# Optimization experiments

Hardware: AMD Instinct MI355X
Metric: run time of the kernel (lower is better)

The kernel has to match this reference:

```python
import jax, jax.numpy as jnp
import numpy as np

N = 100000      # nodes
E = 3200000     # edges (before self-loops)
IN = 1          # input feature dim
H1, C = 4, 8    # layer1: 4 heads x 8 channels; layer2: 1 head x 8 channels
NEG_SLOPE = 0.2


def setup_inputs() -> dict:
    key = jax.random.key(0)
    ks = jax.random.split(key, 10)
    x = jax.random.normal(ks[0], (N, IN), jnp.float32)
    edge_index = jax.random.randint(ks[1], (2, E), 0, N, dtype=jnp.int32)
    # layer 1 params (GATConv(1, 8, heads=4))
    W1 = jax.random.normal(ks[2], (IN, H1 * C), jnp.float32) * 0.5
    a_src1 = jax.random.normal(ks[3], (H1, C), jnp.float32) * 0.5
    a_dst1 = jax.random.normal(ks[4], (H1, C), jnp.float32) * 0.5
    b1 = jnp.zeros((H1 * C,), jnp.float32)
    # layer 2 params (GATConv(32, 8, heads=1))
    W2 = jax.random.normal(ks[5], (H1 * C, C), jnp.float32) * 0.2
    a_src2 = jax.random.normal(ks[6], (1, C), jnp.float32) * 0.5
    a_dst2 = jax.random.normal(ks[7], (1, C), jnp.float32) * 0.5
    b2 = jnp.zeros((C,), jnp.float32)
    return {"x": x, "edge_index": edge_index, "W1": W1, "a_src1": a_src1,
            "a_dst1": a_dst1, "b1": b1, "W2": W2, "a_src2": a_src2,
            "a_dst2": a_dst2, "b2": b2}


def _gat_layer(x, src, dst, W, a_s, a_d, b, heads, ch):
    # Linear transform per head: [N, heads, ch]
    h = (x @ W).reshape(-1, heads, ch)
    # per-node attention logits
    al_s = jnp.einsum('nhc,hc->nh', h, a_s)  # [N, H]
    al_d = jnp.einsum('nhc,hc->nh', h, a_d)  # [N, H]
    # per-edge logits (message src -> dst)
    e = jax.nn.leaky_relu(al_s[src] + al_d[dst], NEG_SLOPE)  # [E', H]
    # segment softmax over incoming edges of each dst node
    m = jax.ops.segment_max(e, dst, num_segments=N)          # [N, H]
    e = jnp.exp(e - m[dst])
    s = jax.ops.segment_sum(e, dst, num_segments=N)          # [N, H]
    alpha = e / s[dst]                                       # [E', H]
    # weighted scatter-add aggregation
    out = jax.ops.segment_sum(h[src] * alpha[:, :, None], dst, num_segments=N)
    return out.reshape(N, heads * ch) + b


def reference(x, edge_index, W1, a_src1, a_dst1, b1, W2, a_src2, a_dst2, b2):
    loops = jnp.arange(N, dtype=edge_index.dtype)
    src = jnp.concatenate([edge_index[0], loops])  # add self-loops (PyG default)
    dst = jnp.concatenate([edge_index[1], loops])
    h = _gat_layer(x, src, dst, W1, a_src1, a_dst1, b1, H1, C)
    h = jax.nn.relu(h)
    out = _gat_layer(h, src, dst, W2, a_src2, a_dst2, b2, 1, C)
    return out
```

## Files before the change

### kernel.cpp

```cpp
#include <hip/hip_runtime.h>
#include <hip/hip_bf16.h>

#define NEG_SLOPE 0.2f
#define CAPS 8192
#define CAPG 8192
#define CAPA 81920


__global__ void init_cc(int* __restrict__ curA, int* __restrict__ curB,
                        const float* __restrict__ W1,
                        const float* __restrict__ as1,
                        const float* __restrict__ ad1,
                        float* __restrict__ consts) {
    int t = threadIdx.x;
    if (t < 8) {
        int h = t & 3;
        const float* a = (t < 4) ? as1 : ad1;
        float s = 0.f;
        #pragma unroll
        for (int c = 0; c < 8; ++c)
            s += W1[h * 8 + c] * a[h * 8 + c];
        consts[t] = s;
    }
    if (t < 64) curA[t] = t * CAPA;
    curB[t] = t << 13;
}

__global__ void scatterA(const int* __restrict__ ei, int* __restrict__ curA,
                         unsigned int* __restrict__ bufA, int E) {
    __shared__ int cnt[64];
    __shared__ int basel[64];
    int t = threadIdx.x;
    int chunk = (E + gridDim.x - 1) / gridDim.x;
    int lo = blockIdx.x * chunk;
    int hi = min(E, lo + chunk);
    const int* dei = ei + E;
    if (t < 64) cnt[t] = 0;
    __syncthreads();
    bool vec = ((E & 3) == 0);
    int lo4 = (lo + 3) & ~3;
    int end4 = hi & ~3;
    if (vec && end4 > lo4) {
        for (int e = lo + t; e < lo4; e += 1024) atomicAdd(&cnt[dei[e] >> 11], 1);
        const int4* dei4 = (const int4*)dei;
        for (int v = (lo4 >> 2) + t; v < (end4 >> 2); v += 1024) {
            int4 d = dei4[v];
            atomicAdd(&cnt[d.x >> 11], 1); atomicAdd(&cnt[d.y >> 11], 1);
            atomicAdd(&cnt[d.z >> 11], 1); atomicAdd(&cnt[d.w >> 11], 1);
        }
        for (int e = end4 + t; e < hi; e += 1024) atomicAdd(&cnt[dei[e] >> 11], 1);
    } else {
        for (int e = lo + t; e < hi; e += 1024) atomicAdd(&cnt[dei[e] >> 11], 1);
    }
    __syncthreads();
    if (t < 64) {
        int c = cnt[t];
        basel[t] = c ? (atomicAdd(&curA[t], c) - t * CAPA) : 0;
        cnt[t] = 0;
    }
    __syncthreads();
    if (vec && end4 > lo4) {
        for (int e = lo + t; e < lo4; e += 1024) {
            int s = ei[e], d = dei[e]; int sp = d >> 11;
            int off = basel[sp] + atomicAdd(&cnt[sp], 1);
            if (off < CAPA) bufA[sp * CAPA + off] = (unsigned)s | ((unsigned)(d & 2047) << 17);
        }
        const int4* sei4 = (const int4*)ei;
        const int4* dei4 = (const int4*)dei;
        for (int v = (lo4 >> 2) + t; v < (end4 >> 2); v += 1024) {
            int4 sv = sei4[v]; int4 dv = dei4[v];
            int s0 = dv.x >> 11, s1 = dv.y >> 11, s2 = dv.z >> 11, s3 = dv.w >> 11;
            int o0 = basel[s0] + atomicAdd(&cnt[s0], 1);
            if (o0 < CAPA) bufA[s0 * CAPA + o0] = (unsigned)sv.x | ((unsigned)(dv.x & 2047) << 17);
            int o1 = basel[s1] + atomicAdd(&cnt[s1], 1);
            if (o1 < CAPA) bufA[s1 * CAPA + o1] = (unsigned)sv.y | ((unsigned)(dv.y & 2047) << 17);
            int o2 = basel[s2] + atomicAdd(&cnt[s2], 1);
            if (o2 < CAPA) bufA[s2 * CAPA + o2] = (unsigned)sv.z | ((unsigned)(dv.z & 2047) << 17);
            int o3 = basel[s3] + atomicAdd(&cnt[s3], 1);
            if (o3 < CAPA) bufA[s3 * CAPA + o3] = (unsigned)sv.w | ((unsigned)(dv.w & 2047) << 17);
        }
        for (int e = end4 + t; e < hi; e += 1024) {
            int s = ei[e], d = dei[e]; int sp = d >> 11;
            int off = basel[sp] + atomicAdd(&cnt[sp], 1);
            if (off < CAPA) bufA[sp * CAPA + off] = (unsigned)s | ((unsigned)(d & 2047) << 17);
        }
    } else {
        for (int e = lo + t; e < hi; e += 1024) {
            int s = ei[e], d = dei[e]; int sp = d >> 11;
            int off = basel[sp] + atomicAdd(&cnt[sp], 1);
            if (off < CAPA) bufA[sp * CAPA + off] = (unsigned)s | ((unsigned)(d & 2047) << 17);
        }
    }
}

__global__ void scatterB(const int* __restrict__ curA, int* __restrict__ curB,
                         const unsigned int* __restrict__ bufA,
                         unsigned int* __restrict__ pairs) {
    __shared__ int cnt[16];
    __shared__ int basel[16];
    int t = threadIdx.x;
    int sp = blockIdx.x >> 3;
    int part = blockIdx.x & 7;
    int base = sp * CAPA;
    int fill = min(curA[sp] - base, CAPA);
    if (fill <= 0) return;
    int lo = (fill * part) >> 3;
    int hi = (fill * (part + 1)) >> 3;
    for (int c0 = lo; c0 < hi; c0 += 8192) {
        int cend = min(hi, c0 + 8192);
        if (t < 16) cnt[t] = 0;
        __syncthreads();
        for (int i = c0 + t; i < cend; i += 1024)
            atomicAdd(&cnt[(bufA[base + i] >> 24) & 15], 1);
        __syncthreads();
        if (t < 16) {
            int c = cnt[t];
            int bkg = (sp << 4) + t;
            basel[t] = c ? (atomicAdd(&curB[bkg], c) - (bkg << 13)) : 0;
            cnt[t] = 0;
        }
        __syncthreads();
        for (int i = c0 + t; i < cend; i += 1024) {
            unsigned p = bufA[base + i];
            int b16 = (p >> 24) & 15;
            int off = basel[b16] + atomicAdd(&cnt[b16], 1);
            if (off < CAPG) pairs[(((sp << 4) + b16) << 13) + off] = p & 0x00FFFFFFu;
        }
        __syncthreads();
    }
}

__global__ __launch_bounds__(512, 8)
void l1_comb(const float* __restrict__ x,
             const int* __restrict__ curB,
             const unsigned int* __restrict__ pairs,
             unsigned int* __restrict__ gsorted, int* __restrict__ bmeta,
             const float* __restrict__ consts,
             const float* __restrict__ W1, const float* __restrict__ b1,
             const float* __restrict__ W2,
             const float* __restrict__ as2, const float* __restrict__ ad2,
             float* __restrict__ h2, float* __restrict__ als2,
             float* __restrict__ ald2, int N) {
    __shared__ unsigned sbuf[CAPS];
    __shared__ int hcnt[128], offs[128], hcur[128];
    __shared__ float xl[128];
    int t = threadIdx.x;
    int bk = blockIdx.x;
    int node0 = bk << 7;
    int nw = min(128, N - node0);
    if (t < 128) xl[t] = (t < nw) ? x[node0 + t] : 0.f;
    float S[4], D[4];
    #pragma unroll
    for (int h = 0; h < 4; ++h) { S[h] = consts[h]; D[h] = consts[4 + h]; }
    int base = bk << 13;
    int clen = min(curB[bk] - base, CAPG);
    int clen6 = min(clen, 6144);
    int g = t >> 2, jj = t & 3;
    unsigned pr[12];
    #pragma unroll
    for (int k = 0; k < 12; ++k) {
        int idx = t + (k << 9);
        pr[k] = (idx < clen6) ? pairs[base + idx] : 0xFFFFFFFFu;
    }
    if (t < 128) hcnt[t] = 0;
    __syncthreads();
    #pragma unroll
    for (int k = 0; k < 12; ++k)
        if (pr[k] != 0xFFFFFFFFu) atomicAdd(&hcnt[pr[k] >> 17], 1);
    for (int idx = 6144 + t; idx < clen; idx += 512)
        atomicAdd(&hcnt[pairs[base + idx] >> 17], 1);
    __syncthreads();
    if (t < 64) {
        int h0 = hcnt[2 * t], h1 = hcnt[2 * t + 1];
        int s = h0 + h1, sc_ = s;
        #pragma unroll
        for (int o = 1; o < 64; o <<= 1) {
            int u = __shfl_up(sc_, o);
            if (t >= o) sc_ += u;
        }
        int excl = sc_ - s;
        offs[2 * t] = excl;          hcur[2 * t] = excl;
        offs[2 * t + 1] = excl + h0; hcur[2 * t + 1] = excl + h0;
    }
    __syncthreads();
    #pragma unroll
    for (int k = 0; k < 12; ++k)
        if (pr[k] != 0xFFFFFFFFu) {
            int loc = atomicAdd(&hcur[pr[k] >> 17], 1);
            sbuf[loc] = pr[k];
        }
    for (int idx = 6144 + t; idx < clen; idx += 512) {
        unsigned p = pairs[base + idx];
        int loc = atomicAdd(&hcur[p >> 17], 1);
        sbuf[loc] = p;
    }
    __syncthreads();
    for (int i = t; i < clen; i += 512) gsorted[base + i] = sbuf[i];
    if (t < 128) bmeta[(bk << 7) + t] = offs[t] | (hcnt[t] << 14);
    float xd = xl[g];
    float sacc[4] = {0.f, 0.f, 0.f, 0.f};
    float tacc[4] = {0.f, 0.f, 0.f, 0.f};
    int st = offs[g], en = st + hcnt[g];
    int i = st + jj;
    while (i + 28 < en) {
        unsigned p0 = sbuf[i],      p1 = sbuf[i + 4],  p2 = sbuf[i + 8],
                 p3 = sbuf[i + 12], p4 = sbuf[i + 16], p5 = sbuf[i + 20],
                 p6 = sbuf[i + 24], p7 = sbuf[i + 28];
        float x0 = x[p0 & 131071u], x1 = x[p1 & 131071u];
        float x2 = x[p2 & 131071u], x3 = x[p3 & 131071u];
        float x4 = x[p4 & 131071u], x5 = x[p5 & 131071u];
        float x6 = x[p6 & 131071u], x7 = x[p7 & 131071u];
        float xs_[8] = {x0, x1, x2, x3, x4, x5, x6, x7};
        #pragma unroll
        for (int q = 0; q < 8; ++q) {
            float xs = xs_[q];
            #pragma unroll
            for (int h = 0; h < 4; ++h) {
                float v = xs * S[h] + xd * D[h];
                v = (v > 0.f) ? v : NEG_SLOPE * v;
                float w = __expf(v);
                sacc[h] += w;
                tacc[h] = fmaf(w, xs, tacc[h]);
            }
        }
        i += 32;
    }
    for (; i < en; i += 4) {
        float xs = x[sbuf[i] & 131071u];
        #pragma unroll
        for (int h = 0; h < 4; ++h) {
            float v = xs * S[h] + xd * D[h];
            v = (v > 0.f) ? v : NEG_SLOPE * v;
            float w = __expf(v);
            sacc[h] += w;
            tacc[h] = fmaf(w, xs, tacc[h]);
        }
    }
    #pragma unroll
    for (int h = 0; h < 4; ++h) {
        sacc[h] += __shfl_xor(sacc[h], 1); sacc[h] += __shfl_xor(sacc[h], 2);
        tacc[h] += __shfl_xor(tacc[h], 1); tacc[h] += __shfl_xor(tacc[h], 2);
    }
    if (jj == 0 && g < nw) {
        int n = node0 + g;
        float xn = xd;
        float o[8];
        #pragma unroll
        for (int c = 0; c < 8; ++c) o[c] = 0.f;
        #pragma unroll
        for (int h = 0; h < 4; ++h) {
            float v = xn * (S[h] + D[h]);
            v = (v > 0.f) ? v : NEG_SLOPE * v;
            float ww = __expf(v);
            float s1 = ww + sacc[h];
            float t1 = ww * xn + tacc[h];
            float tt = t1 / s1;
            #pragma unroll
            for (int c = 0; c < 8; ++c) {
                float rr = fmaxf(tt * W1[h * 8 + c] + b1[h * 8 + c], 0.f);
                #pragma unroll
                for (int c2 = 0; c2 < 8; ++c2) o[c2] += rr * W2[(h * 8 + c) * 8 + c2];
            }
        }
        float as = 0.f, ad = 0.f;
        #pragma unroll
        for (int c = 0; c < 8; ++c) { as += o[c] * as2[c]; ad += o[c] * ad2[c]; }
        float4* hv = (float4*)&h2[(size_t)n * 8];
        hv[0] = make_float4(o[0], o[1], o[2], o[3]);
        hv[1] = make_float4(o[4], o[5], o[6], o[7]);
        als2[n] = as;
        ald2[n] = ad;
    }
}

__global__ __launch_bounds__(512, 8)
void l2_comb(const unsigned int* __restrict__ gsorted,
             const int* __restrict__ bmeta,
             const float* __restrict__ als2, const float* __restrict__ ald2,
             const float* __restrict__ h2, const float* __restrict__ b2,
             float* __restrict__ out, int N) {
    __shared__ float adl[128];
    int t = threadIdx.x;
    int bk = blockIdx.x;
    int node0 = bk << 7;
    int nw = min(128, N - node0);
    if (t < 128) adl[t] = (t < nw) ? ald2[node0 + t] : 0.f;
    __syncthreads();
    int g = t >> 2, j2 = t & 3;
    if (g >= nw) return;
    int base = bk << 13;
    int pk = bmeta[(bk << 7) + g];
    int st = pk & 16383, cgn = pk >> 14;
    const unsigned* run = gsorted + base + st;
    const float2* h2f2 = (const float2*)h2;
    float adv = adl[g];
    float sw = 0.f, acc0 = 0.f, acc1 = 0.f;
    int i = 0;
    while (i + 8 <= cgn) {
        unsigned p0 = run[i],     p1 = run[i + 1], p2 = run[i + 2], p3 = run[i + 3],
                 p4 = run[i + 4], p5 = run[i + 5], p6 = run[i + 6], p7 = run[i + 7];
        int s0 = (int)(p0 & 131071u), s1 = (int)(p1 & 131071u);
        int s2 = (int)(p2 & 131071u), s3 = (int)(p3 & 131071u);
        int s4 = (int)(p4 & 131071u), s5 = (int)(p5 & 131071u);
        int s6 = (int)(p6 & 131071u), s7 = (int)(p7 & 131071u);
        float a0 = als2[s0], a1 = als2[s1], a2 = als2[s2], a3 = als2[s3];
        float a4 = als2[s4], a5 = als2[s5], a6 = als2[s6], a7 = als2[s7];
        float2 h0 = h2f2[s0 * 4 + j2], h1 = h2f2[s1 * 4 + j2];
        float2 h2v = h2f2[s2 * 4 + j2], h3 = h2f2[s3 * 4 + j2];
        float2 h4 = h2f2[s4 * 4 + j2], h5 = h2f2[s5 * 4 + j2];
        float2 h6 = h2f2[s6 * 4 + j2], h7 = h2f2[s7 * 4 + j2];
        float aa[8] = {a0, a1, a2, a3, a4, a5, a6, a7};
        float2 hh[8] = {h0, h1, h2v, h3, h4, h5, h6, h7};
        #pragma unroll
        for (int q = 0; q < 8; ++q) {
            float v = aa[q] + adv;
            v = (v > 0.f) ? v : NEG_SLOPE * v;
            float w = __expf(v);
            sw += w;
            acc0 = fmaf(w, hh[q].x, acc0);
            acc1 = fmaf(w, hh[q].y, acc1);
        }
        i += 8;
    }
    for (; i < cgn; ++i) {
        unsigned p = run[i];
        int s = (int)(p & 131071u);
        float a = als2[s];
        float2 hv = h2f2[s * 4 + j2];
        float v = a + adv;
        v = (v > 0.f) ? v : NEG_SLOPE * v;
        float w = __expf(v);
        sw += w;
        acc0 = fmaf(w, hv.x, acc0);
        acc1 = fmaf(w, hv.y, acc1);
    }
    int n = node0 + g;
    float v = als2[n] + adv;
    v = (v > 0.f) ? v : NEG_SLOPE * v;
    float ww = __expf(v);
    float2 hs = h2f2[n * 4 + j2];
    float inv = 1.f / (sw + ww);
    float2* ov = (float2*)&out[(size_t)n * 8];
    ov[j2] = make_float2((acc0 + ww * hs.x) * inv + b2[2 * j2],
                         (acc1 + ww * hs.y) * inv + b2[2 * j2 + 1]);
}


__global__ void prep_consts(const float* __restrict__ W1,
                            const float* __restrict__ as1,
                            const float* __restrict__ ad1,
                            float* __restrict__ consts) {
    int t = threadIdx.x;
    if (t >= 8) return;
    int h = t & 3;
    const float* a = (t < 4) ? as1 : ad1;
    float s = 0.f;
    #pragma unroll
    for (int c = 0; c < 8; ++c)
        s += W1[h * 8 + c] * a[h * 8 + c];
    consts[t] = s;
}

__global__ void edge_pass1(const int* __restrict__ ei, const float* __restrict__ x,
                           const float* __restrict__ consts,
                           float* __restrict__ s1, float* __restrict__ t1, int E, int N) {
    int e = blockIdx.x * blockDim.x + threadIdx.x;
    if (e >= E + N) return;
    int src, dst;
    if (e < E) { src = ei[e]; dst = ei[E + e]; }
    else       { src = dst = e - E; }
    float xs = x[src], xd = x[dst];
    #pragma unroll
    for (int h = 0; h < 4; ++h) {
        float v = xs * consts[h] + xd * consts[4 + h];
        v = (v > 0.f) ? v : NEG_SLOPE * v;
        float w = __expf(v);
        atomicAdd(&s1[dst * 4 + h], w);
        atomicAdd(&t1[dst * 4 + h], w * xs);
    }
}

__global__ void node_mid(const float* __restrict__ s1, const float* __restrict__ t1,
                         const float* __restrict__ W1, const float* __restrict__ b1,
                         const float* __restrict__ W2,
                         const float* __restrict__ as2, const float* __restrict__ ad2,
                         float* __restrict__ h2, float* __restrict__ als2,
                         float* __restrict__ ald2, int N) {
    int n = blockIdx.x * blockDim.x + threadIdx.x;
    if (n >= N) return;
    float o[8];
    #pragma unroll
    for (int c = 0; c < 8; ++c) o[c] = 0.f;
    #pragma unroll
    for (int h = 0; h < 4; ++h) {
        float t = t1[n * 4 + h] / s1[n * 4 + h];
        #pragma unroll
        for (int c = 0; c < 8; ++c) {
            float r = fmaxf(t * W1[h * 8 + c] + b1[h * 8 + c], 0.f);
            #pragma unroll
            for (int c2 = 0; c2 < 8; ++c2) o[c2] += r * W2[(h * 8 + c) * 8 + c2];
        }
    }
    float as = 0.f, ad = 0.f;
    #pragma unroll
    for (int c = 0; c < 8; ++c) { h2[n * 8 + c] = o[c]; as += o[c] * as2[c]; ad += o[c] * ad2[c]; }
    als2[n] = as; ald2[n] = ad;
}

__global__ void edge_pass2(const int* __restrict__ ei, const float* __restrict__ als2,
                           const float* __restrict__ ald2, const float* __restrict__ h2,
                           float* __restrict__ s2, float* __restrict__ acc2, int E, int N) {
    int e = blockIdx.x * blockDim.x + threadIdx.x;
    if (e >= E + N) return;
    int src, dst;
    if (e < E) { src = ei[e]; dst = ei[E + e]; }
    else       { src = dst = e - E; }
    float v = als2[src] + ald2[dst];
    v = (v > 0.f) ? v : NEG_SLOPE * v;
    float w = __expf(v);
    atomicAdd(&s2[dst], w);
    const float4* hs = (const float4*)&h2[src * 8];
    float4 a = hs[0], bq = hs[1];
    float* acc = &acc2[dst * 8];
    atomicAdd(&acc[0], w * a.x);  atomicAdd(&acc[1], w * a.y);
    atomicAdd(&acc[2], w * a.z);  atomicAdd(&acc[3], w * a.w);
    atomicAdd(&acc[4], w * bq.x); atomicAdd(&acc[5], w * bq.y);
    atomicAdd(&acc[6], w * bq.z); atomicAdd(&acc[7], w * bq.w);
}

__global__ void node_out(const float* __restrict__ s2, const float* __restrict__ acc2,
                         const float* __restrict__ b2, float* __restrict__ out, int N) {
    int i = blockIdx.x * blockDim.x + threadIdx.x;
    if (i >= N * 8) return;
    out[i] = acc2[i] / s2[i >> 3] + b2[i & 7];
}


extern "C" void kernel_launch(void* const* d_in, const int* in_sizes, int n_in,
                              void* d_out, int out_size, void* d_ws, size_t ws_size,
                              hipStream_t stream) {
    const float* x   = (const float*)d_in[0];
    const int*   ei  = (const int*)d_in[1];
    const float* W1  = (const float*)d_in[2];
    const float* as1 = (const float*)d_in[3];
    const float* ad1 = (const float*)d_in[4];
    const float* b1  = (const float*)d_in[5];
    const float* W2  = (const float*)d_in[6];
    const float* as2 = (const float*)d_in[7];
    const float* ad2 = (const float*)d_in[8];
    const float* b2  = (const float*)d_in[9];
    float* out = (float*)d_out;

    const int N = in_sizes[0];
    const int E = in_sizes[1] / 2;
    const int NBK = (N + 127) >> 7;

    float* ws = (float*)d_ws;
    size_t need = ((size_t)16 + 64 + 1024 + 131072 + 10 * (size_t)N
                   + 2 * (size_t)1024 * CAPG + (size_t)64 * CAPA) * sizeof(float);

    if (N <= 131072 && ws_size >= need) {
        float*    consts  = ws;
        int*      curA    = (int*)(ws + 16);
        int*      curB    = curA + 64;
        int*      bmeta   = curB + 1024;
        float*    als2    = (float*)(bmeta + 131072);
        float*    ald2    = als2 + N;
        float*    h2      = ald2 + N;
        unsigned* pairs   = (unsigned*)(h2 + 8 * (size_t)N);
        unsigned* gsorted = pairs + (size_t)1024 * CAPG;
        unsigned* bufA    = gsorted + (size_t)1024 * CAPG;

        init_cc<<<1, 1024, 0, stream>>>(curA, curB, W1, as1, ad1, consts);
        scatterA<<<256, 1024, 0, stream>>>(ei, curA, bufA, E);
        scatterB<<<512, 1024, 0, stream>>>(curA, curB, bufA, pairs);
        l1_comb<<<NBK, 512, 0, stream>>>(x, curB, pairs, gsorted, bmeta, consts,
                                         W1, b1, W2, as2, ad2, h2, als2, ald2, N);
        l2_comb<<<NBK, 512, 0, stream>>>(gsorted, bmeta, als2, ald2, h2, b2, out, N);
    } else {
        float* consts = ws;
        float* s1   = ws + 16;
        float* t1   = s1 + 4 * (size_t)N;
        float* h2   = t1 + 4 * (size_t)N;
        float* als2 = h2 + 8 * (size_t)N;
        float* ald2 = als2 + (size_t)N;
        float* s2   = ald2 + (size_t)N;
        float* acc2 = s2 + (size_t)N;

        hipMemsetAsync(ws, 0, (16 + 8 * (size_t)N) * sizeof(float), stream);
        hipMemsetAsync(s2, 0, 9 * (size_t)N * sizeof(float), stream);
        prep_consts<<<1, 64, 0, stream>>>(W1, as1, ad1, consts);
        int total = E + N;
        edge_pass1<<<(total + 255) / 256, 256, 0, stream>>>(ei, x, consts, s1, t1, E, N);
        node_mid<<<(N + 255) / 256, 256, 0, stream>>>(s1, t1, W1, b1, W2, as2, ad2, h2, als2, ald2, N);
        edge_pass2<<<(total + 255) / 256, 256, 0, stream>>>(ei, als2, ald2, h2, s2, acc2, E, N);
        node_out<<<(N * 8 + 255) / 256, 256, 0, stream>>>(s2, acc2, b2, out, N);
    }
}
```

Baseline: 187.0 us.

## Vectorize pair loads/stores and restructure l2_comb with LDS-staged runs and float4 gathers

In l1_comb, the pair loads and the write-back of sorted pairs now use 128-bit uint4 accesses. In l2_comb, the block's sorted edge run is first copied into shared memory with uint4 loads. Each group of four lanes now splits into two edge streams, each lane gathering a float4 half of the source feature row, and the partial sums are combined with a shuffle. This is meant to cut the number of global memory transactions and per-edge index loads. In exchange it uses 32KB of LDS per block, which may lower occupancy, and it assumes 16-byte alignment.

```diff
diff --git a/kernel.cpp b/kernel.cpp
--- a/kernel.cpp
+++ b/kernel.cpp
@@ -157,10 +157,20 @@
     int clen6 = min(clen, 6144);
     int g = t >> 2, jj = t & 3;
     unsigned pr[12];
-    #pragma unroll
-    for (int k = 0; k < 12; ++k) {
-        int idx = t + (k << 9);
-        pr[k] = (idx < clen6) ? pairs[base + idx] : 0xFFFFFFFFu;
+    const uint4* pairs4 = (const uint4*)(pairs + base);
+    #pragma unroll
+    for (int k = 0; k < 3; ++k) {
+        int w4 = t + (k << 9);
+        int wi = w4 << 2;
+        if (wi + 3 < clen6) {
+            uint4 v = pairs4[w4];
+            pr[4 * k]     = v.x; pr[4 * k + 1] = v.y;
+            pr[4 * k + 2] = v.z; pr[4 * k + 3] = v.w;
+        } else {
+            #pragma unroll
+            for (int m = 0; m < 4; ++m)
+                pr[4 * k + m] = (wi + m < clen6) ? pairs[base + wi + m] : 0xFFFFFFFFu;
+        }
     }
     if (t < 128) hcnt[t] = 0;
     __syncthreads();
@@ -195,7 +205,14 @@
         sbuf[loc] = p;
     }
     __syncthreads();
-    for (int i = t; i < clen; i += 512) gsorted[base + i] = sbuf[i];
+    {
+        int clen4 = clen & ~3;
+        for (int i = t << 2; i < clen4; i += 2048) {
+            uint4 v = *(const uint4*)&sbuf[i];
+            *(uint4*)&gsorted[base + i] = v;
+        }
+        for (int i = clen4 + t; i < clen; i += 512) gsorted[base + i] = sbuf[i];
+    }
     if (t < 128) bmeta[(bk << 7) + t] = offs[t] | (hcnt[t] << 14);
     float xd = xl[g];
     float sacc[4] = {0.f, 0.f, 0.f, 0.f};
@@ -274,75 +291,104 @@
 }
 
 __global__ __launch_bounds__(512, 8)
-void l2_comb(const unsigned int* __restrict__ gsorted,
+void l2_comb(const int* __restrict__ curB,
+             const unsigned int* __restrict__ gsorted,
              const int* __restrict__ bmeta,
              const float* __restrict__ als2, const float* __restrict__ ald2,
              const float* __restrict__ h2, const float* __restrict__ b2,
              float* __restrict__ out, int N) {
+    __shared__ unsigned runl[CAPS];
     __shared__ float adl[128];
     int t = threadIdx.x;
     int bk = blockIdx.x;
     int node0 = bk << 7;
     int nw = min(128, N - node0);
     if (t < 128) adl[t] = (t < nw) ? ald2[node0 + t] : 0.f;
-    __syncthreads();
-    int g = t >> 2, j2 = t & 3;
+    int base = bk << 13;
+    int clen = min(curB[bk] - base, CAPG);
+    {
+        int clen4 = clen & ~3;
+        const uint4* g4 = (const uint4*)(gsorted + base);
+        for (int i = t << 2; i < clen4; i += 2048) {
+            uint4 v = g4[i >> 2];
+            *(uint4*)&runl[i] = v;
+        }
+        for (int i = clen4 + t; i < clen; i += 512) runl[i] = gsorted[base + i];
+    }
+    __syncthreads();
+    int g = t >> 2, j = t & 3;
+    int jh = j & 1;
+    int jp = j >> 1;
     if (g >= nw) return;
-    int base = bk << 13;
     int pk = bmeta[(bk << 7) + g];
     int st = pk & 16383, cgn = pk >> 14;
-    const unsigned* run = gsorted + base + st;
-    const float2* h2f2 = (const float2*)h2;
+    const unsigned* run = runl + st;
     float adv = adl[g];
-    float sw = 0.f, acc0 = 0.f, acc1 = 0.f;
-    int i = 0;
-    while (i + 8 <= cgn) {
-        unsigned p0 = run[i],     p1 = run[i + 1], p2 = run[i + 2], p3 = run[i + 3],
-                 p4 = run[i + 4], p5 = run[i + 5], p6 = run[i + 6], p7 = run[i + 7];
-        int s0 = (int)(p0 & 131071u), s1 = (int)(p1 & 131071u);
-        int s2 = (int)(p2 & 131071u), s3 = (int)(p3 & 131071u);
-        int s4 = (int)(p4 & 131071u), s5 = (int)(p5 & 131071u);
-        int s6 = (int)(p6 & 131071u), s7 = (int)(p7 & 131071u);
-        float a0 = als2[s0], a1 = als2[s1], a2 = als2[s2], a3 = als2[s3];
-        float a4 = als2[s4], a5 = als2[s5], a6 = als2[s6], a7 = als2[s7];
-        float2 h0 = h2f2[s0 * 4 + j2], h1 = h2f2[s1 * 4 + j2];
-        float2 h2v = h2f2[s2 * 4 + j2], h3 = h2f2[s3 * 4 + j2];
-        float2 h4 = h2f2[s4 * 4 + j2], h5 = h2f2[s5 * 4 + j2];
-        float2 h6 = h2f2[s6 * 4 + j2], h7 = h2f2[s7 * 4 + j2];
-        float aa[8] = {a0, a1, a2, a3, a4, a5, a6, a7};
-        float2 hh[8] = {h0, h1, h2v, h3, h4, h5, h6, h7};
-        #pragma unroll
-        for (int q = 0; q < 8; ++q) {
+    int co = jh << 2;
+    float4 acc = make_float4(0.f, 0.f, 0.f, 0.f);
+    float sw = 0.f;
+    int k = 0;
+    while (2 * k + 8 <= cgn) {
+        unsigned q0 = run[2 * k + jp];
+        unsigned q1 = run[2 * k + 2 + jp];
+        unsigned q2 = run[2 * k + 4 + jp];
+        unsigned q3 = run[2 * k + 6 + jp];
+        size_t r0 = (size_t)(q0 & 131071u) * 8 + co;
+        size_t r1 = (size_t)(q1 & 131071u) * 8 + co;
+        size_t r2 = (size_t)(q2 & 131071u) * 8 + co;
+        size_t r3 = (size_t)(q3 & 131071u) * 8 + co;
+        float4 h0 = *(const float4*)&h2[r0];
+        float4 h1 = *(const float4*)&h2[r1];
+        float4 h2v = *(const float4*)&h2[r2];
+        float4 h3 = *(const float4*)&h2[r3];
+        float a0 = als2[q0 & 131071u], a1 = als2[q1 & 131071u];
+        float a2 = als2[q2 & 131071u], a3 = als2[q3 & 131071u];
+        float aa[4] = {a0, a1, a2, a3};
+        float4 hh[4] = {h0, h1, h2v, h3};
+        #pragma unroll
+        for (int q = 0; q < 4; ++q) {
             float v = aa[q] + adv;
             v = (v > 0.f) ? v : NEG_SLOPE * v;
             float w = __expf(v);
             sw += w;
-            acc0 = fmaf(w, hh[q].x, acc0);
-            acc1 = fmaf(w, hh[q].y, acc1);
-        }
-        i += 8;
-    }
-    for (; i < cgn; ++i) {
-        unsigned p = run[i];
-        int s = (int)(p & 131071u);
-        float a = als2[s];
-        float2 hv = h2f2[s * 4 + j2];
+            acc.x = fmaf(w, hh[q].x, acc.x);
+            acc.y = fmaf(w, hh[q].y, acc.y);
+            acc.z = fmaf(w, hh[q].z, acc.z);
+            acc.w = fmaf(w, hh[q].w, acc.w);
+        }
+        k += 4;
+    }
+    for (; 2 * k + jp < cgn; ++k) {
+        unsigned q = run[2 * k + jp];
+        size_t r = (size_t)(q & 131071u) * 8 + co;
+        float4 hq = *(const float4*)&h2[r];
+        float a = als2[q & 131071u];
         float v = a + adv;
         v = (v > 0.f) ? v : NEG_SLOPE * v;
         float w = __expf(v);
         sw += w;
-        acc0 = fmaf(w, hv.x, acc0);
-        acc1 = fmaf(w, hv.y, acc1);
-    }
+        acc.x = fmaf(w, hq.x, acc.x);
+        acc.y = fmaf(w, hq.y, acc.y);
+        acc.z = fmaf(w, hq.z, acc.z);
+        acc.w = fmaf(w, hq.w, acc.w);
+    }
+    acc.x += __shfl_xor(acc.x, 2); acc.y += __shfl_xor(acc.y, 2);
+    acc.z += __shfl_xor(acc.z, 2); acc.w += __shfl_xor(acc.w, 2);
+    sw += __shfl_xor(sw, 2);
     int n = node0 + g;
     float v = als2[n] + adv;
     v = (v > 0.f) ? v : NEG_SLOPE * v;
     float ww = __expf(v);
-    float2 hs = h2f2[n * 4 + j2];
+    float4 hs = *(const float4*)&h2[(size_t)n * 8 + co];
     float inv = 1.f / (sw + ww);
-    float2* ov = (float2*)&out[(size_t)n * 8];
-    ov[j2] = make_float2((acc0 + ww * hs.x) * inv + b2[2 * j2],
-                         (acc1 + ww * hs.y) * inv + b2[2 * j2 + 1]);
+    if (jp == 0) {
+        float4 bb = *(const float4*)&b2[co];
+        *(float4*)&out[(size_t)n * 8 + co] = make_float4(
+            (acc.x + ww * hs.x) * inv + bb.x,
+            (acc.y + ww * hs.y) * inv + bb.y,
+            (acc.z + ww * hs.z) * inv + bb.z,
+            (acc.w + ww * hs.w) * inv + bb.w);
+    }
 }
 
 
@@ -476,7 +522,7 @@
         scatterB<<<512, 1024, 0, stream>>>(curA, curB, bufA, pairs);
         l1_comb<<<NBK, 512, 0, stream>>>(x, curB, pairs, gsorted, bmeta, consts,
                                          W1, b1, W2, as2, ad2, h2, als2, ald2, N);
-        l2_comb<<<NBK, 512, 0, stream>>>(gsorted, bmeta, als2, ald2, h2, b2, out, N);
+        l2_comb<<<NBK, 512, 0, stream>>>(curB, gsorted, bmeta, als2, ald2, h2, b2, out, N);
     } else {
         float* consts = ws;
         float* s1   = ws + 16;
```

New measurement: 179.2 us, median of 3. 1.04x faster.
